# Optimization experiments

Hardware: AMD Instinct MI355X
Metric: run time of the kernel (lower is better)

Reference implementation:

```python
import jax, jax.numpy as jnp
import numpy as np

D = 768; H = 12; L = 6; B = 8; S = 256; DH = D // H
_SCALE = 1.0 / float(np.sqrt(D))
_SCALE_FFN2 = 1.0 / float(np.sqrt(4 * D))


def _ln(x, g, b):
    m = jnp.mean(x, axis=-1, keepdims=True)
    v = jnp.mean((x - m) ** 2, axis=-1, keepdims=True)
    return (x - m) / jnp.sqrt(v + 1e-12) * g + b


def _mhsa(q_in, k_in, v_in, w, bias, mask, scale):
    # w: [3, D, D], bias: [3, D]; mask: [B, S_k]
    def proj(t, W, b):
        return (t @ W + b).reshape(t.shape[0], t.shape[1], H, DH).transpose(0, 2, 1, 3)
    q = proj(q_in, w[0], bias[0])
    k = proj(k_in, w[1], bias[1])
    v = proj(v_in, w[2], bias[2])
    s = jnp.einsum('bhqd,bhkd->bhqk', q, k) * scale
    s = s - 10000.0 * (1.0 - mask[:, None, None, :].astype(s.dtype))
    p = jax.nn.softmax(s, axis=-1)
    h = jnp.einsum('bhqk,bhkd->bhqd', p, v)
    return h.transpose(0, 2, 1, 3).reshape(q_in.shape[0], q_in.shape[1], D)


def _ffn(x, w1, b1, w2, b2):
    return jax.nn.gelu(x @ w1 + b1, approximate=False) @ w2 + b2


def setup_inputs() -> dict:
    key = jax.random.key(0)
    ks = jax.random.split(key, 16)
    inp = {
        'x': jax.random.normal(ks[0], (B, S, D), jnp.float32),
        'y': jax.random.normal(ks[1], (B, S, D), jnp.float32),
        'x_mask': jnp.ones((B, S), jnp.int32),
        'y_mask': jnp.ones((B, S), jnp.int32),
        'ax_w': jax.random.normal(ks[2], (L, 3, D, D), jnp.float32) * _SCALE,
        'ax_b': jnp.zeros((L, 3, D), jnp.float32),
        'cx_w': jax.random.normal(ks[3], (L, 3, D, D), jnp.float32) * _SCALE,
        'cx_b': jnp.zeros((L, 3, D), jnp.float32),
        'fx_w1': jax.random.normal(ks[4], (L, D, 4 * D), jnp.float32) * _SCALE,
        'fx_b1': jnp.zeros((L, 4 * D), jnp.float32),
        'fx_w2': jax.random.normal(ks[5], (L, 4 * D, D), jnp.float32) * _SCALE_FFN2,
        'fx_b2': jnp.zeros((L, D), jnp.float32),
        'ay_w': jax.random.normal(ks[6], (L, 3, D, D), jnp.float32) * _SCALE,
        'ay_b': jnp.zeros((L, 3, D), jnp.float32),
        'cy_w': jax.random.normal(ks[7], (L, 3, D, D), jnp.float32) * _SCALE,
        'cy_b': jnp.zeros((L, 3, D), jnp.float32),
        'fy_w1': jax.random.normal(ks[8], (L, D, 4 * D), jnp.float32) * _SCALE,
        'fy_b1': jnp.zeros((L, 4 * D), jnp.float32),
        'fy_w2': jax.random.normal(ks[9], (L, 4 * D, D), jnp.float32) * _SCALE_FFN2,
        'fy_b2': jnp.zeros((L, D), jnp.float32),
        'lnx_g': jnp.ones((3, D), jnp.float32),
        'lnx_b': jnp.zeros((3, D), jnp.float32),
        'lny_g': jnp.ones((3, D), jnp.float32),
        'lny_b': jnp.zeros((3, D), jnp.float32),
    }
    return inp


def reference(x, y, x_mask, y_mask, ax_w, ax_b, cx_w, cx_b, fx_w1, fx_b1, fx_w2, fx_b2,
              ay_w, ay_b, cy_w, cy_b, fy_w1, fy_b1, fy_w2, fy_b2,
              lnx_g, lnx_b, lny_g, lny_b):
    inv_sqrt_dh = 1.0 / float(np.sqrt(DH))
    params = dict(ax_w=ax_w, ax_b=ax_b, cx_w=cx_w, cx_b=cx_b,
                  fx_w1=fx_w1, fx_b1=fx_b1, fx_w2=fx_w2, fx_b2=fx_b2,
                  ay_w=ay_w, ay_b=ay_b, cy_w=cy_w, cy_b=cy_b,
                  fy_w1=fy_w1, fy_b1=fy_b1, fy_w2=fy_w2, fy_b2=fy_b2)

    def layer(carry, p):
        xc, yc = carry
        xc = _ln(xc + _mhsa(xc, xc, xc, p['ax_w'], p['ax_b'], x_mask, inv_sqrt_dh), lnx_g[0], lnx_b[0])
        yc = _ln(yc + _mhsa(yc, yc, yc, p['ay_w'], p['ay_b'], y_mask, inv_sqrt_dh), lny_g[0], lny_b[0])
        xc = _ln(xc + _mhsa(xc, yc, yc, p['cx_w'], p['cx_b'], y_mask, inv_sqrt_dh), lnx_g[1], lnx_b[1])
        yc = _ln(yc + _mhsa(yc, xc, xc, p['cy_w'], p['cy_b'], x_mask, inv_sqrt_dh), lny_g[1], lny_b[1])
        xc = _ln(xc + _ffn(xc, p['fx_w1'], p['fx_b1'], p['fx_w2'], p['fx_b2']), lnx_g[2], lnx_b[2])
        yc = _ln(yc + _ffn(yc, p['fy_w1'], p['fy_b1'], p['fy_w2'], p['fy_b2']), lny_g[2], lny_b[2])
        return (xc, yc), None

    (x, y), _ = jax.lax.scan(layer, (x, y), params)
    return jnp.stack([x, y])  # [2, B, S, D]
```

## Files before the change

### kernel.cpp

```cpp
#include <hip/hip_runtime.h>
#include <math.h>

constexpr int D = 768;
constexpr int H = 12;
constexpr int L = 6;
constexpr int B = 8;
constexpr int S = 256;
constexpr int DH = 64;
constexpr int M = B * S;
constexpr int D4 = 4 * D;

typedef _Float16 v2h __attribute__((ext_vector_type(2)));
typedef _Float16 v4h __attribute__((ext_vector_type(4)));
typedef _Float16 v8h __attribute__((ext_vector_type(8)));
typedef __fp16 f16x2 __attribute__((ext_vector_type(2)));
typedef float v4f __attribute__((ext_vector_type(4)));

__device__ inline void cvt_split(float x, float y, v2h& hi, v2h& lo) {
    f16x2 h = __builtin_amdgcn_cvt_pkrtz(x, y);
    float rx = x - (float)h[0];
    float ry = y - (float)h[1];
    f16x2 l = __builtin_amdgcn_cvt_pkrtz(rx, ry);
    hi = __builtin_bit_cast(v2h, h);
    lo = __builtin_bit_cast(v2h, l);
}

__global__ __launch_bounds__(256) void gemm_mfma(
    const float* __restrict__ Aq0, const float* __restrict__ Akv0,
    const float* __restrict__ W0,  const float* __restrict__ bias0, float* __restrict__ C0,
    const float* __restrict__ Aq1, const float* __restrict__ Akv1,
    const float* __restrict__ W1,  const float* __restrict__ bias1, float* __restrict__ C1,
    int qsplit, int K, int N, int n_per_mat, int act)
{
    const int z = blockIdx.z;
    const float* __restrict__ Aq  = z ? Aq1  : Aq0;
    const float* __restrict__ Akv = z ? Akv1 : Akv0;
    const float* __restrict__ Wb  = z ? W1   : W0;
    const float* __restrict__ bias = z ? bias1 : bias0;
    float* __restrict__ C = z ? C1 : C0;

    const int n0 = blockIdx.x * 128;
    const int m0 = blockIdx.y * 128;
    const float* __restrict__ A = (n0 < qsplit) ? Aq : Akv;
    const int sub = n0 / n_per_mat;
    const int nc0 = n0 - sub * n_per_mat;
    const float* __restrict__ W = Wb + (size_t)sub * K * n_per_mat;

    const int tid = threadIdx.x;
    const int lane = tid & 63;
    const int wave = tid >> 6;
    const int wm = (wave & 1) * 64;
    const int wn = (wave >> 1) * 64;

    __shared__ _Float16 sm[4 * 128 * 40];
    _Float16* Ah = sm;
    _Float16* Al = sm + 128 * 40;
    _Float16* Bh = sm + 2 * 128 * 40;
    _Float16* Bl = sm + 3 * 128 * 40;

    v4f acc[4][4];
    #pragma unroll
    for (int i = 0; i < 4; ++i)
        #pragma unroll
        for (int j = 0; j < 4; ++j)
            acc[i][j] = (v4f){0.f, 0.f, 0.f, 0.f};

    const int ar = tid >> 3;
    const int ac = (tid & 7) * 4;
    const int bn = tid & 127;
    const int bk0 = (tid >> 7) * 16;

    const int fm = lane & 15;
    const int fk = (lane >> 4) * 8;

    float4 av[4];
    float bv[16];
    #pragma unroll
    for (int i = 0; i < 4; ++i)
        av[i] = *(const float4*)(A + (size_t)(m0 + ar + 32 * i) * K + ac);
    #pragma unroll
    for (int j = 0; j < 16; ++j)
        bv[j] = W[(size_t)(bk0 + j) * n_per_mat + nc0 + bn];

    for (int k0 = 0; k0 < K; k0 += 32) {
        float4 av2[4];
        float bv2[16];
        if (k0 + 32 < K) {
            #pragma unroll
            for (int i = 0; i < 4; ++i)
                av2[i] = *(const float4*)(A + (size_t)(m0 + ar + 32 * i) * K + k0 + 32 + ac);
            #pragma unroll
            for (int j = 0; j < 16; ++j)
                bv2[j] = W[(size_t)(k0 + 32 + bk0 + j) * n_per_mat + nc0 + bn];
        }

        __syncthreads();

        #pragma unroll
        for (int i = 0; i < 4; ++i) {
            v2h h0, l0, h1, l1;
            cvt_split(av[i].x, av[i].y, h0, l0);
            cvt_split(av[i].z, av[i].w, h1, l1);
            v4h hh, ll;
            hh[0] = h0[0]; hh[1] = h0[1]; hh[2] = h1[0]; hh[3] = h1[1];
            ll[0] = l0[0]; ll[1] = l0[1]; ll[2] = l1[0]; ll[3] = l1[1];
            *(v4h*)&Ah[(ar + 32 * i) * 40 + ac] = hh;
            *(v4h*)&Al[(ar + 32 * i) * 40 + ac] = ll;
        }
        {
            v8h bha, bhb, bla, blb;
            #pragma unroll
            for (int j = 0; j < 4; ++j) {
                v2h h, l;
                cvt_split(bv[2 * j], bv[2 * j + 1], h, l);
                bha[2 * j] = h[0]; bha[2 * j + 1] = h[1];
                bla[2 * j] = l[0]; bla[2 * j + 1] = l[1];
            }
            #pragma unroll
            for (int j = 0; j < 4; ++j) {
                v2h h, l;
                cvt_split(bv[8 + 2 * j], bv[8 + 2 * j + 1], h, l);
                bhb[2 * j] = h[0]; bhb[2 * j + 1] = h[1];
                blb[2 * j] = l[0]; blb[2 * j + 1] = l[1];
            }
            *(v8h*)&Bh[bn * 40 + bk0] = bha;
            *(v8h*)&Bh[bn * 40 + bk0 + 8] = bhb;
            *(v8h*)&Bl[bn * 40 + bk0] = bla;
            *(v8h*)&Bl[bn * 40 + bk0 + 8] = blb;
        }
        __syncthreads();

        v8h fah[4], fal[4], fbh[4], fbl[4];
        #pragma unroll
        for (int i = 0; i < 4; ++i) {
            fah[i] = *(v8h*)&Ah[(wm + i * 16 + fm) * 40 + fk];
            fal[i] = *(v8h*)&Al[(wm + i * 16 + fm) * 40 + fk];
        }
        #pragma unroll
        for (int j = 0; j < 4; ++j) {
            fbh[j] = *(v8h*)&Bh[(wn + j * 16 + fm) * 40 + fk];
            fbl[j] = *(v8h*)&Bl[(wn + j * 16 + fm) * 40 + fk];
        }
        #pragma unroll
        for (int i = 0; i < 4; ++i)
            #pragma unroll
            for (int j = 0; j < 4; ++j) {
                acc[i][j] = __builtin_amdgcn_mfma_f32_16x16x32_f16(fah[i], fbh[j], acc[i][j], 0, 0, 0);
                acc[i][j] = __builtin_amdgcn_mfma_f32_16x16x32_f16(fah[i], fbl[j], acc[i][j], 0, 0, 0);
                acc[i][j] = __builtin_amdgcn_mfma_f32_16x16x32_f16(fal[i], fbh[j], acc[i][j], 0, 0, 0);
            }

        #pragma unroll
        for (int i = 0; i < 4; ++i) av[i] = av2[i];
        #pragma unroll
        for (int j = 0; j < 16; ++j) bv[j] = bv2[j];
    }

    const int er = (lane >> 4) * 4;
    const int ec = lane & 15;
    #pragma unroll
    for (int j = 0; j < 4; ++j) {
        const int col = n0 + wn + j * 16 + ec;
        const float bs = bias[col];
        #pragma unroll
        for (int i = 0; i < 4; ++i) {
            #pragma unroll
            for (int r = 0; r < 4; ++r) {
                const int row = m0 + wm + i * 16 + er + r;
                float v = acc[i][j][r] + bs;
                if (act == 1)
                    v = 0.5f * v * (1.0f + erff(v * 0.7071067811865476f));
                C[(size_t)row * N + col] = v;
            }
        }
    }
}

__global__ __launch_bounds__(256) void attn_kernel(
    const float* __restrict__ qkv0, const int* __restrict__ mask0, float* __restrict__ hout0,
    const float* __restrict__ qkv1, const int* __restrict__ mask1, float* __restrict__ hout1)
{
    const float* __restrict__ qkv = blockIdx.z ? qkv1 : qkv0;
    const int* __restrict__ mask = blockIdx.z ? mask1 : mask0;
    float* __restrict__ hout = blockIdx.z ? hout1 : hout0;

    const int blk = blockIdx.x;
    const int qt = blk & 3;
    const int bh = blk >> 2;
    const int head = bh % H;
    const int b = bh / H;
    const int tid = threadIdx.x;
    const int wave = tid >> 6;
    const int lane = tid & 63;
    const int qloc = lane & 15;
    const int rg = lane >> 4;

    __shared__ _Float16 KVh[64 * 72];
    __shared__ _Float16 KVl[64 * 72];
    __shared__ _Float16 Ph[4][16 * 72];
    __shared__ _Float16 Pl[4][16 * 72];
    __shared__ float mpen[256];

    mpen[tid] = -10000.0f * (1.0f - (float)mask[b * S + tid]);

    const int qrow = b * S + qt * 64 + wave * 16 + qloc;
    const float* qptr = qkv + (size_t)qrow * 2304 + head * DH + rg * 8;
    v8h qh[2], ql[2];
    #pragma unroll
    for (int ks = 0; ks < 2; ++ks) {
        float4 a = *(const float4*)(qptr + ks * 32);
        float4 c = *(const float4*)(qptr + ks * 32 + 4);
        v2h h, l;
        v8h hh, ll;
        cvt_split(a.x, a.y, h, l); hh[0] = h[0]; hh[1] = h[1]; ll[0] = l[0]; ll[1] = l[1];
        cvt_split(a.z, a.w, h, l); hh[2] = h[0]; hh[3] = h[1]; ll[2] = l[0]; ll[3] = l[1];
        cvt_split(c.x, c.y, h, l); hh[4] = h[0]; hh[5] = h[1]; ll[4] = l[0]; ll[5] = l[1];
        cvt_split(c.z, c.w, h, l); hh[6] = h[0]; hh[7] = h[1]; ll[6] = l[0]; ll[7] = l[1];
        qh[ks] = hh; ql[ks] = ll;
    }

    v4f acc_s[16];
    #pragma unroll
    for (int i = 0; i < 16; ++i) acc_s[i] = (v4f){0.f, 0.f, 0.f, 0.f};

    const float* kbase = qkv + 768 + head * DH;
    const float* vbase = qkv + 1536 + head * DH;

    const int skey = tid & 63;
    const int sseg = (tid >> 6) * 16;
    #pragma unroll
    for (int t = 0; t < 4; ++t) {
        __syncthreads();
        {
            const float* src = kbase + (size_t)(b * S + t * 64 + skey) * 2304 + sseg;
            float4 a = ((const float4*)src)[0];
            float4 c = ((const float4*)src)[1];
            float4 e = ((const float4*)src)[2];
            float4 f = ((const float4*)src)[3];
            v2h h, l;
            v8h hA, lA, hB, lB;
            cvt_split(a.x, a.y, h, l); hA[0] = h[0]; hA[1] = h[1]; lA[0] = l[0]; lA[1] = l[1];
            cvt_split(a.z, a.w, h, l); hA[2] = h[0]; hA[3] = h[1]; lA[2] = l[0]; lA[3] = l[1];
            cvt_split(c.x, c.y, h, l); hA[4] = h[0]; hA[5] = h[1]; lA[4] = l[0]; lA[5] = l[1];
            cvt_split(c.z, c.w, h, l); hA[6] = h[0]; hA[7] = h[1]; lA[6] = l[0]; lA[7] = l[1];
            cvt_split(e.x, e.y, h, l); hB[0] = h[0]; hB[1] = h[1]; lB[0] = l[0]; lB[1] = l[1];
            cvt_split(e.z, e.w, h, l); hB[2] = h[0]; hB[3] = h[1]; lB[2] = l[0]; lB[3] = l[1];
            cvt_split(f.x, f.y, h, l); hB[4] = h[0]; hB[5] = h[1]; lB[4] = l[0]; lB[5] = l[1];
            cvt_split(f.z, f.w, h, l); hB[6] = h[0]; hB[7] = h[1]; lB[6] = l[0]; lB[7] = l[1];
            *(v8h*)&KVh[skey * 72 + sseg] = hA;
            *(v8h*)&KVh[skey * 72 + sseg + 8] = hB;
            *(v8h*)&KVl[skey * 72 + sseg] = lA;
            *(v8h*)&KVl[skey * 72 + sseg + 8] = lB;
        }
        __syncthreads();
        #pragma unroll
        for (int sub = 0; sub < 4; ++sub) {
            v8h kh[2], kl[2];
            #pragma unroll
            for (int ks = 0; ks < 2; ++ks) {
                kh[ks] = *(v8h*)&KVh[(sub * 16 + qloc) * 72 + ks * 32 + rg * 8];
                kl[ks] = *(v8h*)&KVl[(sub * 16 + qloc) * 72 + ks * 32 + rg * 8];
            }
            v4f acc = acc_s[t * 4 + sub];
            #pragma unroll
            for (int ks = 0; ks < 2; ++ks) {
                acc = __builtin_amdgcn_mfma_f32_16x16x32_f16(kh[ks], qh[ks], acc, 0, 0, 0);
                acc = __builtin_amdgcn_mfma_f32_16x16x32_f16(kh[ks], ql[ks], acc, 0, 0, 0);
                acc = __builtin_amdgcn_mfma_f32_16x16x32_f16(kl[ks], qh[ks], acc, 0, 0, 0);
            }
            acc_s[t * 4 + sub] = acc;
        }
    }

    float mx = -3.0e38f;
    #pragma unroll
    for (int mt = 0; mt < 16; ++mt) {
        float4 mp = *(const float4*)&mpen[mt * 16 + rg * 4];
        v4f s = acc_s[mt];
        s[0] = s[0] * 0.125f + mp.x;
        s[1] = s[1] * 0.125f + mp.y;
        s[2] = s[2] * 0.125f + mp.z;
        s[3] = s[3] * 0.125f + mp.w;
        acc_s[mt] = s;
        mx = fmaxf(mx, fmaxf(fmaxf(s[0], s[1]), fmaxf(s[2], s[3])));
    }
    mx = fmaxf(mx, __shfl_xor(mx, 16, 64));
    mx = fmaxf(mx, __shfl_xor(mx, 32, 64));
    float sum = 0.f;
    #pragma unroll
    for (int mt = 0; mt < 16; ++mt) {
        v4f s = acc_s[mt];
        s[0] = __expf(s[0] - mx);
        s[1] = __expf(s[1] - mx);
        s[2] = __expf(s[2] - mx);
        s[3] = __expf(s[3] - mx);
        acc_s[mt] = s;
        sum += (s[0] + s[1]) + (s[2] + s[3]);
    }
    sum += __shfl_xor(sum, 16, 64);
    sum += __shfl_xor(sum, 32, 64);
    const float inv = 1.0f / sum;

    v4f acc_o[4];
    #pragma unroll
    for (int j = 0; j < 4; ++j) acc_o[j] = (v4f){0.f, 0.f, 0.f, 0.f};

    const int vk4 = (tid & 15) * 4;
    const int vd4 = (tid >> 4) * 4;
    #pragma unroll
    for (int t = 0; t < 4; ++t) {
        __syncthreads();
        #pragma unroll
        for (int sub = 0; sub < 4; ++sub) {
            v4f p = acc_s[t * 4 + sub];
            v2h h01, l01, h23, l23;
            cvt_split(p[0], p[1], h01, l01);
            cvt_split(p[2], p[3], h23, l23);
            *(v2h*)&Ph[wave][qloc * 72 + sub * 16 + rg * 4] = h01;
            *(v2h*)&Ph[wave][qloc * 72 + sub * 16 + rg * 4 + 2] = h23;
            *(v2h*)&Pl[wave][qloc * 72 + sub * 16 + rg * 4] = l01;
            *(v2h*)&Pl[wave][qloc * 72 + sub * 16 + rg * 4 + 2] = l23;
        }
        {
            v4h rh[4], rl[4];
            #pragma unroll
            for (int i = 0; i < 4; ++i) {
                const float4 vv = *(const float4*)(vbase + (size_t)(b * S + t * 64 + vk4 + i) * 2304 + vd4);
                v2h h0, l0, h1, l1;
                cvt_split(vv.x, vv.y, h0, l0);
                cvt_split(vv.z, vv.w, h1, l1);
                rh[0][i] = h0[0]; rh[1][i] = h0[1]; rh[2][i] = h1[0]; rh[3][i] = h1[1];
                rl[0][i] = l0[0]; rl[1][i] = l0[1]; rl[2][i] = l1[0]; rl[3][i] = l1[1];
            }
            #pragma unroll
            for (int j = 0; j < 4; ++j) {
                *(v4h*)&KVh[(vd4 + j) * 72 + vk4] = rh[j];
                *(v4h*)&KVl[(vd4 + j) * 72 + vk4] = rl[j];
            }
        }
        __syncthreads();
        v8h pah[2], pal[2];
        #pragma unroll
        for (int ks = 0; ks < 2; ++ks) {
            pah[ks] = *(v8h*)&Ph[wave][qloc * 72 + ks * 32 + rg * 8];
            pal[ks] = *(v8h*)&Pl[wave][qloc * 72 + ks * 32 + rg * 8];
        }
        #pragma unroll
        for (int j = 0; j < 4; ++j) {
            v4f acc = acc_o[j];
            #pragma unroll
            for (int ks = 0; ks < 2; ++ks) {
                v8h vbh = *(v8h*)&KVh[(j * 16 + qloc) * 72 + ks * 32 + rg * 8];
                v8h vbl = *(v8h*)&KVl[(j * 16 + qloc) * 72 + ks * 32 + rg * 8];
                acc = __builtin_amdgcn_mfma_f32_16x16x32_f16(pah[ks], vbh, acc, 0, 0, 0);
                acc = __builtin_amdgcn_mfma_f32_16x16x32_f16(pah[ks], vbl, acc, 0, 0, 0);
                acc = __builtin_amdgcn_mfma_f32_16x16x32_f16(pal[ks], vbh, acc, 0, 0, 0);
            }
            acc_o[j] = acc;
        }
    }

    #pragma unroll
    for (int r = 0; r < 4; ++r) {
        const float invr = __shfl(inv, rg * 4 + r, 64);
        const size_t row = (size_t)(b * S + qt * 64 + wave * 16 + rg * 4 + r);
        #pragma unroll
        for (int j = 0; j < 4; ++j)
            hout[row * D + head * DH + j * 16 + qloc] = acc_o[j][r] * invr;
    }
}

__global__ __launch_bounds__(256) void ln_res_kernel(
    float* __restrict__ x0, const float* __restrict__ h0,
    const float* __restrict__ g0, const float* __restrict__ bb0,
    float* __restrict__ x1, const float* __restrict__ h1,
    const float* __restrict__ g1, const float* __restrict__ bb1)
{
    float* __restrict__ x = blockIdx.y ? x1 : x0;
    const float* __restrict__ h = blockIdx.y ? h1 : h0;
    const float* __restrict__ g = blockIdx.y ? g1 : g0;
    const float* __restrict__ bb = blockIdx.y ? bb1 : bb0;

    const int row = blockIdx.x;
    const int tid = threadIdx.x;
    const int wave = tid >> 6;
    const int lane = tid & 63;
    __shared__ float red[4];

    float v[3];
    #pragma unroll
    for (int i = 0; i < 3; ++i) {
        int c = tid + 256 * i;
        v[i] = x[(size_t)row * D + c] + h[(size_t)row * D + c];
    }
    float s = v[0] + v[1] + v[2];
    #pragma unroll
    for (int o = 32; o > 0; o >>= 1) s += __shfl_xor(s, o, 64);
    if (lane == 0) red[wave] = s;
    __syncthreads();
    const float mean = (red[0] + red[1] + red[2] + red[3]) * (1.0f / 768.0f);

    float qs = 0.f;
    #pragma unroll
    for (int i = 0; i < 3; ++i) { float d = v[i] - mean; qs += d * d; }
    #pragma unroll
    for (int o = 32; o > 0; o >>= 1) qs += __shfl_xor(qs, o, 64);
    __syncthreads();
    if (lane == 0) red[wave] = qs;
    __syncthreads();
    const float var = (red[0] + red[1] + red[2] + red[3]) * (1.0f / 768.0f);
    const float rstd = rsqrtf(var + 1e-12f);

    #pragma unroll
    for (int i = 0; i < 3; ++i) {
        int c = tid + 256 * i;
        x[(size_t)row * D + c] = (v[i] - mean) * rstd * g[c] + bb[c];
    }
}

extern "C" void kernel_launch(void* const* d_in, const int* in_sizes, int n_in,
                              void* d_out, int out_size, void* d_ws, size_t ws_size,
                              hipStream_t stream)
{
    const float* x    = (const float*)d_in[0];
    const float* y    = (const float*)d_in[1];
    const int*   xm   = (const int*)d_in[2];
    const int*   ym   = (const int*)d_in[3];
    const float* ax_w = (const float*)d_in[4];
    const float* ax_b = (const float*)d_in[5];
    const float* cx_w = (const float*)d_in[6];
    const float* cx_b = (const float*)d_in[7];
    const float* fx_w1 = (const float*)d_in[8];
    const float* fx_b1 = (const float*)d_in[9];
    const float* fx_w2 = (const float*)d_in[10];
    const float* fx_b2 = (const float*)d_in[11];
    const float* ay_w = (const float*)d_in[12];
    const float* ay_b = (const float*)d_in[13];
    const float* cy_w = (const float*)d_in[14];
    const float* cy_b = (const float*)d_in[15];
    const float* fy_w1 = (const float*)d_in[16];
    const float* fy_b1 = (const float*)d_in[17];
    const float* fy_w2 = (const float*)d_in[18];
    const float* fy_b2 = (const float*)d_in[19];
    const float* lnx_g = (const float*)d_in[20];
    const float* lnx_b = (const float*)d_in[21];
    const float* lny_g = (const float*)d_in[22];
    const float* lny_b = (const float*)d_in[23];

    float* xc = (float*)d_out;
    float* yc = xc + (size_t)M * D;

    const size_t need = ((size_t)2 * M * D4 + (size_t)2 * M * D) * sizeof(float);
    const bool big = ws_size >= need;
    float* ws0 = (float*)d_ws;
    float* qkvx = ws0;
    float* qkvy = big ? ws0 + (size_t)M * D4 : ws0;
    float* hbx = ws0 + (big ? (size_t)2 * M * D4 : (size_t)M * D4);
    float* hby = big ? hbx + (size_t)M * D : hbx;

    (void)hipMemcpyAsync(xc, x, (size_t)M * D * sizeof(float), hipMemcpyDeviceToDevice, stream);
    (void)hipMemcpyAsync(yc, y, (size_t)M * D * sizeof(float), hipMemcpyDeviceToDevice, stream);

    const dim3 blk(256);

    auto qkv_gemm = [&](const float* aq0, const float* akv0, const float* w0, const float* bi0, float* c0,
                        const float* aq1, const float* akv1, const float* w1, const float* bi1, float* c1,
                        int nz) {
        gemm_mfma<<<dim3(2304 / 128, M / 128, nz), blk, 0, stream>>>(
            aq0, akv0, w0, bi0, c0, aq1, akv1, w1, bi1, c1, 768, D, 2304, 768, 0);
    };
    auto ffn1_gemm = [&](const float* a0, const float* w0, const float* bi0, float* c0,
                         const float* a1, const float* w1, const float* bi1, float* c1, int nz) {
        gemm_mfma<<<dim3(D4 / 128, M / 128, nz), blk, 0, stream>>>(
            a0, a0, w0, bi0, c0, a1, a1, w1, bi1, c1, 0, D, D4, D4, 1);
    };
    auto ffn2_gemm = [&](const float* a0, const float* w0, const float* bi0, float* c0,
                         const float* a1, const float* w1, const float* bi1, float* c1, int nz) {
        gemm_mfma<<<dim3(D / 128, M / 128, nz), blk, 0, stream>>>(
            a0, a0, w0, bi0, c0, a1, a1, w1, bi1, c1, 0, D4, D, D, 0);
    };
    auto attn = [&](const float* q0, const int* m0_, float* h0,
                    const float* q1, const int* m1_, float* h1, int nz) {
        attn_kernel<<<dim3(B * H * 4, 1, nz), blk, 0, stream>>>(q0, m0_, h0, q1, m1_, h1);
    };
    auto ln = [&](float* x0, const float* h0, const float* g0, const float* b0,
                  float* x1, const float* h1, const float* g1, const float* b1, int ny) {
        ln_res_kernel<<<dim3(M, ny), blk, 0, stream>>>(x0, h0, g0, b0, x1, h1, g1, b1);
    };

    for (int l = 0; l < L; ++l) {
        const size_t wo = (size_t)l * 3 * D * D;
        const size_t bo = (size_t)l * 3 * D;
        const size_t f1o = (size_t)l * D * D4;
        const size_t f1bo = (size_t)l * D4;
        const size_t f2o = (size_t)l * D4 * D;
        const size_t f2bo = (size_t)l * D;

        if (big) {
            qkv_gemm(xc, xc, ax_w + wo, ax_b + bo, qkvx,
                     yc, yc, ay_w + wo, ay_b + bo, qkvy, 2);
            attn(qkvx, xm, hbx, qkvy, ym, hby, 2);
            ln(xc, hbx, lnx_g, lnx_b, yc, hby, lny_g, lny_b, 2);
            qkv_gemm(xc, yc, cx_w + wo, cx_b + bo, qkvx,
                     xc, yc, cx_w + wo, cx_b + bo, qkvx, 1);
            attn(qkvx, ym, hbx, qkvx, ym, hbx, 1);
            ln(xc, hbx, lnx_g + D, lnx_b + D, xc, hbx, lnx_g + D, lnx_b + D, 1);
            qkv_gemm(yc, xc, cy_w + wo, cy_b + bo, qkvy,
                     yc, xc, cy_w + wo, cy_b + bo, qkvy, 1);
            attn(qkvy, xm, hby, qkvy, xm, hby, 1);
            ln(yc, hby, lny_g + D, lny_b + D, yc, hby, lny_g + D, lny_b + D, 1);
            ffn1_gemm(xc, fx_w1 + f1o, fx_b1 + f1bo, qkvx,
                      yc, fy_w1 + f1o, fy_b1 + f1bo, qkvy, 2);
            ffn2_gemm(qkvx, fx_w2 + f2o, fx_b2 + f2bo, hbx,
                      qkvy, fy_w2 + f2o, fy_b2 + f2bo, hby, 2);
            ln(xc, hbx, lnx_g + 2 * D, lnx_b + 2 * D,
               yc, hby, lny_g + 2 * D, lny_b + 2 * D, 2);
        } else {
            qkv_gemm(xc, xc, ax_w + wo, ax_b + bo, qkvx, xc, xc, ax_w + wo, ax_b + bo, qkvx, 1);
            attn(qkvx, xm, hbx, qkvx, xm, hbx, 1);
            ln(xc, hbx, lnx_g, lnx_b, xc, hbx, lnx_g, lnx_b, 1);
            qkv_gemm(yc, yc, ay_w + wo, ay_b + bo, qkvy, yc, yc, ay_w + wo, ay_b + bo, qkvy, 1);
            attn(qkvy, ym, hby, qkvy, ym, hby, 1);
            ln(yc, hby, lny_g, lny_b, yc, hby, lny_g, lny_b, 1);
            qkv_gemm(xc, yc, cx_w + wo, cx_b + bo, qkvx, xc, yc, cx_w + wo, cx_b + bo, qkvx, 1);
            attn(qkvx, ym, hbx, qkvx, ym, hbx, 1);
            ln(xc, hbx, lnx_g + D, lnx_b + D, xc, hbx, lnx_g + D, lnx_b + D, 1);
            qkv_gemm(yc, xc, cy_w + wo, cy_b + bo, qkvy, yc, xc, cy_w + wo, cy_b + bo, qkvy, 1);
            attn(qkvy, xm, hby, qkvy, xm, hby, 1);
            ln(yc, hby, lny_g + D, lny_b + D, yc, hby, lny_g + D, lny_b + D, 1);
            ffn1_gemm(xc, fx_w1 + f1o, fx_b1 + f1bo, qkvx, xc, fx_w1 + f1o, fx_b1 + f1bo, qkvx, 1);
            ffn2_gemm(qkvx, fx_w2 + f2o, fx_b2 + f2bo, hbx, qkvx, fx_w2 + f2o, fx_b2 + f2bo, hbx, 1);
            ln(xc, hbx, lnx_g + 2 * D, lnx_b + 2 * D, xc, hbx, lnx_g + 2 * D, lnx_b + 2 * D, 1);
            ffn1_gemm(yc, fy_w1 + f1o, fy_b1 + f1bo, qkvy, yc, fy_w1 + f1o, fy_b1 + f1bo, qkvy, 1);
            ffn2_gemm(qkvy, fy_w2 + f2o, fy_b2 + f2bo, hby, qkvy, fy_w2 + f2o, fy_b2 + f2bo, hby, 1);
            ln(yc, hby, lny_g + 2 * D, lny_b + 2 * D, yc, hby, lny_g + 2 * D, lny_b + 2 * D, 1);
        }
    }
}
```

Baseline: 3.728 ms.

## Split-K the FFN2 GEMM with atomic accumulation and move prefetch after LDS sync

The FFN down-projection (K=3072, N=768) is split into four K-chunks launched as separate blocks, and each block atomically adds its partial result into an output buffer zeroed by a memset. This raises the block count for a GEMM that otherwise has few output tiles and a long K loop, in exchange for atomic traffic, a memset and nondeterministic summation order. The global prefetch of the next tile is also moved from before the first barrier to after the LDS store barrier, which changes register lifetimes and the overlap of loads with MFMA work.

```diff
diff --git a/kernel.cpp b/kernel.cpp
--- a/kernel.cpp
+++ b/kernel.cpp
@@ -30,21 +30,26 @@
     const float* __restrict__ W0,  const float* __restrict__ bias0, float* __restrict__ C0,
     const float* __restrict__ Aq1, const float* __restrict__ Akv1,
     const float* __restrict__ W1,  const float* __restrict__ bias1, float* __restrict__ C1,
-    int qsplit, int K, int N, int n_per_mat, int act)
+    int qsplit, int Kstride, int kchunk, int N, int n_per_mat, int nblks, int act, int atomic)
 {
     const int z = blockIdx.z;
     const float* __restrict__ Aq  = z ? Aq1  : Aq0;
     const float* __restrict__ Akv = z ? Akv1 : Akv0;
     const float* __restrict__ Wb  = z ? W1   : W0;
-    const float* __restrict__ bias = z ? bias1 : bias0;
+    const float* __restrict__ biasz = z ? bias1 : bias0;
     float* __restrict__ C = z ? C1 : C0;
 
-    const int n0 = blockIdx.x * 128;
+    const int bx = blockIdx.x;
+    const int nb = bx % nblks;
+    const int kpart = bx / nblks;
+    const int n0 = nb * 128;
     const int m0 = blockIdx.y * 128;
-    const float* __restrict__ A = (n0 < qsplit) ? Aq : Akv;
+    const float* __restrict__ A = ((n0 < qsplit) ? Aq : Akv) + (size_t)kpart * kchunk;
     const int sub = n0 / n_per_mat;
     const int nc0 = n0 - sub * n_per_mat;
-    const float* __restrict__ W = Wb + (size_t)sub * K * n_per_mat;
+    const float* __restrict__ W = Wb + (size_t)sub * Kstride * n_per_mat
+                                     + (size_t)kpart * kchunk * n_per_mat;
+    const float* __restrict__ bias = (kpart == 0) ? biasz : nullptr;
 
     const int tid = threadIdx.x;
     const int lane = tid & 63;
@@ -73,27 +78,16 @@
     const int fm = lane & 15;
     const int fk = (lane >> 4) * 8;
 
-    float4 av[4];
-    float bv[16];
+    float4 av[4], av2[4];
+    float bv[16], bv2[16];
     #pragma unroll
     for (int i = 0; i < 4; ++i)
-        av[i] = *(const float4*)(A + (size_t)(m0 + ar + 32 * i) * K + ac);
+        av[i] = *(const float4*)(A + (size_t)(m0 + ar + 32 * i) * Kstride + ac);
     #pragma unroll
     for (int j = 0; j < 16; ++j)
         bv[j] = W[(size_t)(bk0 + j) * n_per_mat + nc0 + bn];
 
-    for (int k0 = 0; k0 < K; k0 += 32) {
-        float4 av2[4];
-        float bv2[16];
-        if (k0 + 32 < K) {
-            #pragma unroll
-            for (int i = 0; i < 4; ++i)
-                av2[i] = *(const float4*)(A + (size_t)(m0 + ar + 32 * i) * K + k0 + 32 + ac);
-            #pragma unroll
-            for (int j = 0; j < 16; ++j)
-                bv2[j] = W[(size_t)(k0 + 32 + bk0 + j) * n_per_mat + nc0 + bn];
-        }
-
+    for (int k0 = 0; k0 < kchunk; k0 += 32) {
         __syncthreads();
 
         #pragma unroll
@@ -130,6 +124,15 @@
         }
         __syncthreads();
 
+        if (k0 + 32 < kchunk) {
+            #pragma unroll
+            for (int i = 0; i < 4; ++i)
+                av2[i] = *(const float4*)(A + (size_t)(m0 + ar + 32 * i) * Kstride + k0 + 32 + ac);
+            #pragma unroll
+            for (int j = 0; j < 16; ++j)
+                bv2[j] = W[(size_t)(k0 + 32 + bk0 + j) * n_per_mat + nc0 + bn];
+        }
+
         v8h fah[4], fal[4], fbh[4], fbl[4];
         #pragma unroll
         for (int i = 0; i < 4; ++i) {
@@ -161,7 +164,7 @@
     #pragma unroll
     for (int j = 0; j < 4; ++j) {
         const int col = n0 + wn + j * 16 + ec;
-        const float bs = bias[col];
+        const float bs = bias ? bias[col] : 0.0f;
         #pragma unroll
         for (int i = 0; i < 4; ++i) {
             #pragma unroll
@@ -170,7 +173,10 @@
                 float v = acc[i][j][r] + bs;
                 if (act == 1)
                     v = 0.5f * v * (1.0f + erff(v * 0.7071067811865476f));
-                C[(size_t)row * N + col] = v;
+                if (atomic)
+                    atomicAdd(&C[(size_t)row * N + col], v);
+                else
+                    C[(size_t)row * N + col] = v;
             }
         }
     }
@@ -462,22 +468,32 @@
     (void)hipMemcpyAsync(yc, y, (size_t)M * D * sizeof(float), hipMemcpyDeviceToDevice, stream);
 
     const dim3 blk(256);
+    constexpr int KSPLIT = 4;
 
     auto qkv_gemm = [&](const float* aq0, const float* akv0, const float* w0, const float* bi0, float* c0,
                         const float* aq1, const float* akv1, const float* w1, const float* bi1, float* c1,
                         int nz) {
         gemm_mfma<<<dim3(2304 / 128, M / 128, nz), blk, 0, stream>>>(
-            aq0, akv0, w0, bi0, c0, aq1, akv1, w1, bi1, c1, 768, D, 2304, 768, 0);
+            aq0, akv0, w0, bi0, c0, aq1, akv1, w1, bi1, c1,
+            768, D, D, 2304, 768, 2304 / 128, 0, 0);
     };
     auto ffn1_gemm = [&](const float* a0, const float* w0, const float* bi0, float* c0,
                          const float* a1, const float* w1, const float* bi1, float* c1, int nz) {
         gemm_mfma<<<dim3(D4 / 128, M / 128, nz), blk, 0, stream>>>(
-            a0, a0, w0, bi0, c0, a1, a1, w1, bi1, c1, 0, D, D4, D4, 1);
+            a0, a0, w0, bi0, c0, a1, a1, w1, bi1, c1,
+            0, D, D, D4, D4, D4 / 128, 1, 0);
     };
-    auto ffn2_gemm = [&](const float* a0, const float* w0, const float* bi0, float* c0,
-                         const float* a1, const float* w1, const float* bi1, float* c1, int nz) {
+    auto ffn2_gemm_split = [&](const float* a0, const float* w0, const float* bi0, float* c0,
+                               const float* a1, const float* w1, const float* bi1, float* c1, int nz) {
+        gemm_mfma<<<dim3((D / 128) * KSPLIT, M / 128, nz), blk, 0, stream>>>(
+            a0, a0, w0, bi0, c0, a1, a1, w1, bi1, c1,
+            0, D4, D4 / KSPLIT, D, D, D / 128, 0, 1);
+    };
+    auto ffn2_gemm_seq = [&](const float* a0, const float* w0, const float* bi0, float* c0,
+                             const float* a1, const float* w1, const float* bi1, float* c1, int nz) {
         gemm_mfma<<<dim3(D / 128, M / 128, nz), blk, 0, stream>>>(
-            a0, a0, w0, bi0, c0, a1, a1, w1, bi1, c1, 0, D4, D, D, 0);
+            a0, a0, w0, bi0, c0, a1, a1, w1, bi1, c1,
+            0, D4, D4, D, D, D / 128, 0, 0);
     };
     auto attn = [&](const float* q0, const int* m0_, float* h0,
                     const float* q1, const int* m1_, float* h1, int nz) {
@@ -511,8 +527,9 @@
             ln(yc, hby, lny_g + D, lny_b + D, yc, hby, lny_g + D, lny_b + D, 1);
             ffn1_gemm(xc, fx_w1 + f1o, fx_b1 + f1bo, qkvx,
                       yc, fy_w1 + f1o, fy_b1 + f1bo, qkvy, 2);
-            ffn2_gemm(qkvx, fx_w2 + f2o, fx_b2 + f2bo, hbx,
-                      qkvy, fy_w2 + f2o, fy_b2 + f2bo, hby, 2);
+            (void)hipMemsetAsync(hbx, 0, (size_t)2 * M * D * sizeof(float), stream);
+            ffn2_gemm_split(qkvx, fx_w2 + f2o, fx_b2 + f2bo, hbx,
+                            qkvy, fy_w2 + f2o, fy_b2 + f2bo, hby, 2);
             ln(xc, hbx, lnx_g + 2 * D, lnx_b + 2 * D,
                yc, hby, lny_g + 2 * D, lny_b + 2 * D, 2);
         } else {
@@ -529,10 +546,10 @@
             attn(qkvy, xm, hby, qkvy, xm, hby, 1);
             ln(yc, hby, lny_g + D, lny_b + D, yc, hby, lny_g + D, lny_b + D, 1);
             ffn1_gemm(xc, fx_w1 + f1o, fx_b1 + f1bo, qkvx, xc, fx_w1 + f1o, fx_b1 + f1bo, qkvx, 1);
-            ffn2_gemm(qkvx, fx_w2 + f2o, fx_b2 + f2bo, hbx, qkvx, fx_w2 + f2o, fx_b2 + f2bo, hbx, 1);
+            ffn2_gemm_seq(qkvx, fx_w2 + f2o, fx_b2 + f2bo, hbx, qkvx, fx_w2 + f2o, fx_b2 + f2bo, hbx, 1);
             ln(xc, hbx, lnx_g + 2 * D, lnx_b + 2 * D, xc, hbx, lnx_g + 2 * D, lnx_b + 2 * D, 1);
             ffn1_gemm(yc, fy_w1 + f1o, fy_b1 + f1bo, qkvy, yc, fy_w1 + f1o, fy_b1 + f1bo, qkvy, 1);
-            ffn2_gemm(qkvy, fy_w2 + f2o, fy_b2 + f2bo, hby, qkvy, fy_w2 + f2o, fy_b2 + f2bo, hby, 1);
+            ffn2_gemm_seq(qkvy, fy_w2 + f2o, fy_b2 + f2bo, hby, qkvy, fy_w2 + f2o, fy_b2 + f2bo, hby, 1);
             ln(yc, hby, lny_g + 2 * D, lny_b + 2 * D, yc, hby, lny_g + 2 * D, lny_b + 2 * D, 1);
         }
     }
```

Measured after the change: 3.026 ms. 1.23x faster.
